# Kernel tuning notes

Hardware: AMD Instinct MI355X
Metric: run time of the kernel (lower is better)

The kernel has to match this reference:

```python
import jax, jax.numpy as jnp
import numpy as np

N_EMBD = 1024
N_HEAD = 16
R = 16
SCALING = 1.0 / 16.0  # loralib default lora_alpha=1, scaling = alpha/r


def lora_linear(x, W, b, A, B):
    # loralib: y = x @ W.T + b + (x @ A.T) @ B.T * scaling
    return x @ W.T + b + (x @ A.T) @ B.T * SCALING


def setup_inputs() -> dict:
    key = jax.random.key(0)
    ks = jax.random.split(key, 16)
    B, T, S, C = 8, 1024, 256, N_EMBD
    std = 0.02
    return {
        "x": jax.random.normal(ks[0], (B, T, C), jnp.float32),
        "feature": jax.random.normal(ks[1], (B, S, C), jnp.float32),
        # c_attn (q projection)
        "Wq": jax.random.normal(ks[2], (C, C), jnp.float32) * std,
        "bq": jnp.zeros((C,), jnp.float32),
        "Aq": jax.random.normal(ks[3], (R, C), jnp.float32) * std,
        "Bq": jnp.zeros((C, R), jnp.float32),
        # feature_attn (kv projection)
        "Wf": jax.random.normal(ks[4], (2 * C, C), jnp.float32) * std,
        "bf": jnp.zeros((2 * C,), jnp.float32),
        "Af": jax.random.normal(ks[5], (R, C), jnp.float32) * std,
        "Bf": jnp.zeros((2 * C, R), jnp.float32),
        # c_proj
        "Wp": jax.random.normal(ks[6], (C, C), jnp.float32) * std,
        "bp": jnp.zeros((C,), jnp.float32),
        "Ap": jax.random.normal(ks[7], (R, C), jnp.float32) * std,
        "Bp": jnp.zeros((C, R), jnp.float32),
    }


def reference(x, feature, Wq, bq, Aq, Bq, Wf, bf, Af, Bf, Wp, bp, Ap, Bp):
    Bsz, T, C = x.shape
    S = feature.shape[1]
    H = N_HEAD
    D = C // H

    q = lora_linear(x, Wq, bq, Aq, Bq).reshape(Bsz, T, H, D).transpose(0, 2, 1, 3)
    kv = lora_linear(feature, Wf, bf, Af, Bf)
    k, v = kv[..., :C], kv[..., C:]
    k = k.reshape(Bsz, S, H, D).transpose(0, 2, 1, 3)
    v = v.reshape(Bsz, S, H, D).transpose(0, 2, 1, 3)

    att = jnp.einsum("bhtd,bhsd->bhts", q, k) * (1.0 / np.sqrt(D))
    mask = jnp.tril(jnp.ones((T, S), bool))  # bias[:, :, :T, :S]
    att = jnp.where(mask, att, -jnp.inf)
    att = jax.nn.softmax(att, axis=-1)

    y = jnp.einsum("bhts,bhsd->bhtd", att, v)
    y = y.transpose(0, 2, 1, 3).reshape(Bsz, T, C)
    return lora_linear(y, Wp, bp, Ap, Bp)
```

## Files before the change

kernel.cpp:

```cpp
#include <hip/hip_runtime.h>
#include <hip/hip_bf16.h>
#include <stdint.h>
#include <stddef.h>

typedef __hip_bfloat16 bf16;
typedef __attribute__((ext_vector_type(8))) short short8;
typedef __attribute__((ext_vector_type(4))) float floatx4;

__device__ __forceinline__ void async_load16(const bf16* g, bf16* l) {
#if defined(__has_builtin) && __has_builtin(__builtin_amdgcn_global_load_lds)
  __builtin_amdgcn_global_load_lds((__attribute__((address_space(1))) void*)g,
                                   (__attribute__((address_space(3))) void*)l,
                                   16, 0, 0);
#else
  *(short8*)l = *(const short8*)g;
#endif
}

__device__ __forceinline__ int wave_detect_f32(const unsigned short* __restrict__ xr) {
  const int lane = threadIdx.x & 63;
  const unsigned short u = xr[lane];
  const int e = (u >> 7) & 0xFF;
  const unsigned long long m = __ballot(e >= 0x93);
  return (__popcll(m) > 5) ? 1 : 0;
}

__device__ __forceinline__ float ldf(const void* p, int i, int flg) {
  return flg ? ((const float*)p)[i] : __bfloat162float(((const bf16*)p)[i]);
}

struct PrepArgs {
  const void *x, *ft, *bq, *bf, *bp;
  const void *Wq, *Aq, *Bq, *Wf, *Af, *Bf, *Wp, *Ap, *Bp;
  bf16 *cx, *cft, *cbq, *cbf, *cbp, *weffq, *wefff, *weffp;
};

__device__ __forceinline__ void canon4(const void* src, bf16* dst, int i4, int flg) {
  if (flg) {
    const float4 v = ((const float4*)src)[i4];
    dst[i4 * 4 + 0] = __float2bfloat16(v.x);
    dst[i4 * 4 + 1] = __float2bfloat16(v.y);
    dst[i4 * 4 + 2] = __float2bfloat16(v.z);
    dst[i4 * 4 + 3] = __float2bfloat16(v.w);
  } else {
    ((uint2*)dst)[i4] = ((const uint2*)src)[i4];
  }
}

__device__ __forceinline__ void weff1(const void* W, const void* Bm, const void* Am,
                                      bf16* dst, int idx, int flg) {
  const int n = idx >> 10, k = idx & 1023;
  float acc = 0.f;
#pragma unroll
  for (int r = 0; r < 16; ++r)
    acc += ldf(Bm, n * 16 + r, flg) * ldf(Am, r * 1024 + k, flg);
  dst[idx] = __float2bfloat16(ldf(W, idx, flg) + 0.0625f * acc);
}

__global__ __launch_bounds__(256) void prep_kernel(PrepArgs a) {
  const int flg = wave_detect_f32((const unsigned short*)a.x);
  const int bid = blockIdx.x, tid = threadIdx.x;
  if (bid < 8192) {
    canon4(a.x, a.cx, bid * 256 + tid, flg);
  } else if (bid < 10240) {
    canon4(a.ft, a.cft, (bid - 8192) * 256 + tid, flg);
  } else if (bid < 10241) {
    canon4(a.bq, a.cbq, tid, flg);
  } else if (bid < 10243) {
    canon4(a.bf, a.cbf, (bid - 10241) * 256 + tid, flg);
  } else if (bid < 10244) {
    canon4(a.bp, a.cbp, tid, flg);
  } else if (bid < 14340) {
    weff1(a.Wq, a.Bq, a.Aq, a.weffq, (bid - 10244) * 256 + tid, flg);
  } else if (bid < 22532) {
    weff1(a.Wf, a.Bf, a.Af, a.wefff, (bid - 14340) * 256 + tid, flg);
  } else {
    weff1(a.Wp, a.Bp, a.Ap, a.weffp, (bid - 22532) * 256 + tid, flg);
  }
}

__global__ __launch_bounds__(256) void gemm_qkv(
    const bf16* __restrict__ cx, const bf16* __restrict__ cft,
    const bf16* __restrict__ weffq, const bf16* __restrict__ wefff,
    const bf16* __restrict__ cbq, const bf16* __restrict__ cbf,
    bf16* __restrict__ qws, bf16* __restrict__ kws, bf16* __restrict__ vtws) {
  __shared__ __align__(16) bf16 sA[128 * 32];
  __shared__ __align__(16) bf16 sB[128 * 32];
  const int bid = blockIdx.x, tid = threadIdx.x;
  const int K = 1024;
  int mode, bm, bn;
  const bf16 *A, *Bt, *bias;
  if (bid < 512) {
    mode = 0; A = cx; Bt = weffq; bias = cbq;
    bm = (((bid & 7) << 3) | ((bid >> 3) & 7)) * 128;
    bn = (bid >> 6) * 128;
  } else {
    const int b2 = bid - 512;
    mode = 1; A = cft; Bt = wefff; bias = cbf;
    bm = (((b2 & 7) << 1) | ((b2 >> 3) & 1)) * 128;
    bn = (b2 >> 4) * 128;
  }
  const int srow = tid >> 2;
  const int scol = ((tid & 3) ^ (srow & 3)) << 3;
  const bf16* ga0 = A + (size_t)(bm + srow) * K + scol;
  const bf16* ga1 = ga0 + (size_t)64 * K;
  const bf16* gb0 = Bt + (size_t)(bn + srow) * K + scol;
  const bf16* gb1 = gb0 + (size_t)64 * K;
  bf16* lA0 = sA + tid * 8;
  bf16* lA1 = sA + 2048 + tid * 8;
  bf16* lB0 = sB + tid * 8;
  bf16* lB1 = sB + 2048 + tid * 8;
  const int wave = tid >> 6, lane = tid & 63;
  const int wm = (wave >> 1) << 6, wn = (wave & 1) << 6;
  const int lrow = lane & 15, quad = lane >> 4;
  const int swz = ((quad ^ (lrow & 3)) << 3);

  const floatx4 zero4 = {0.f, 0.f, 0.f, 0.f};
  floatx4 acc[4][4];
#pragma unroll
  for (int i = 0; i < 4; ++i)
#pragma unroll
    for (int j = 0; j < 4; ++j) acc[i][j] = zero4;

  for (int k0 = 0; k0 < K; k0 += 32) {
    async_load16(ga0, lA0);
    async_load16(ga1, lA1);
    async_load16(gb0, lB0);
    async_load16(gb1, lB1);
    ga0 += 32; ga1 += 32; gb0 += 32; gb1 += 32;
    __syncthreads();
    short8 af[4], bfr[4];
#pragma unroll
    for (int i = 0; i < 4; ++i) {
      af[i]  = *(const short8*)(sA + (wm + i * 16 + lrow) * 32 + swz);
      bfr[i] = *(const short8*)(sB + (wn + i * 16 + lrow) * 32 + swz);
    }
#pragma unroll
    for (int i = 0; i < 4; ++i)
#pragma unroll
      for (int j = 0; j < 4; ++j)
        acc[i][j] = __builtin_amdgcn_mfma_f32_16x16x32_bf16(af[i], bfr[j], acc[i][j], 0, 0, 0);
    __syncthreads();
  }

#pragma unroll
  for (int i = 0; i < 4; ++i) {
    const int mbase = bm + wm + i * 16 + quad * 4;
#pragma unroll
    for (int j = 0; j < 4; ++j) {
      const int n = bn + wn + j * 16 + lrow;
      const float bv = __bfloat162float(bias[n]);
#pragma unroll
      for (int r = 0; r < 4; ++r) {
        const int m = mbase + r;
        const bf16 hval = __float2bfloat16(acc[i][j][r] + bv);
        if (mode == 0) {
          const int b = m >> 10, t = m & 1023, hh = n >> 6, d = n & 63;
          qws[(((size_t)(b * 16 + hh)) * 1024 + t) * 64 + d] = hval;
        } else {
          const int b = m >> 8, s = m & 255;
          if (n < 1024) {
            const int hh = n >> 6, d = n & 63;
            kws[(((size_t)(b * 16 + hh)) * 256 + s) * 64 + d] = hval;
          } else {
            const int nn = n - 1024, hh = nn >> 6, d = nn & 63;
            vtws[(((size_t)(b * 16 + hh)) * 64 + d) * 256 + s] = hval;
          }
        }
      }
    }
  }
}

__global__ __launch_bounds__(256) void gemm_out(
    const bf16* __restrict__ A, const bf16* __restrict__ Bt,
    const bf16* __restrict__ bias, void* __restrict__ out0,
    const unsigned short* __restrict__ xraw) {
  __shared__ __align__(16) bf16 sA[128 * 32];
  __shared__ __align__(16) bf16 sB[128 * 32];
  const int bid = blockIdx.x, tid = threadIdx.x;
  const int K = 1024, N = 1024;
  const int bm = (((bid & 7) << 3) | ((bid >> 3) & 7)) * 128;
  const int bn = (bid >> 6) * 128;
  const int srow = tid >> 2;
  const int scol = ((tid & 3) ^ (srow & 3)) << 3;
  const bf16* ga0 = A + (size_t)(bm + srow) * K + scol;
  const bf16* ga1 = ga0 + (size_t)64 * K;
  const bf16* gb0 = Bt + (size_t)(bn + srow) * K + scol;
  const bf16* gb1 = gb0 + (size_t)64 * K;
  bf16* lA0 = sA + tid * 8;
  bf16* lA1 = sA + 2048 + tid * 8;
  bf16* lB0 = sB + tid * 8;
  bf16* lB1 = sB + 2048 + tid * 8;
  const int wave = tid >> 6, lane = tid & 63;
  const int wm = (wave >> 1) << 6, wn = (wave & 1) << 6;
  const int lrow = lane & 15, quad = lane >> 4;
  const int swz = ((quad ^ (lrow & 3)) << 3);

  const floatx4 zero4 = {0.f, 0.f, 0.f, 0.f};
  floatx4 acc[4][4];
#pragma unroll
  for (int i = 0; i < 4; ++i)
#pragma unroll
    for (int j = 0; j < 4; ++j) acc[i][j] = zero4;

  for (int k0 = 0; k0 < K; k0 += 32) {
    async_load16(ga0, lA0);
    async_load16(ga1, lA1);
    async_load16(gb0, lB0);
    async_load16(gb1, lB1);
    ga0 += 32; ga1 += 32; gb0 += 32; gb1 += 32;
    __syncthreads();
    short8 af[4], bfr[4];
#pragma unroll
    for (int i = 0; i < 4; ++i) {
      af[i]  = *(const short8*)(sA + (wm + i * 16 + lrow) * 32 + swz);
      bfr[i] = *(const short8*)(sB + (wn + i * 16 + lrow) * 32 + swz);
    }
#pragma unroll
    for (int i = 0; i < 4; ++i)
#pragma unroll
      for (int j = 0; j < 4; ++j)
        acc[i][j] = __builtin_amdgcn_mfma_f32_16x16x32_bf16(af[i], bfr[j], acc[i][j], 0, 0, 0);
    __syncthreads();
  }

  const int flg = wave_detect_f32(xraw);
#pragma unroll
  for (int i = 0; i < 4; ++i) {
    const int mbase = bm + wm + i * 16 + quad * 4;
#pragma unroll
    for (int j = 0; j < 4; ++j) {
      const int n = bn + wn + j * 16 + lrow;
      const float bv = __bfloat162float(bias[n]);
#pragma unroll
      for (int r = 0; r < 4; ++r) {
        const int m = mbase + r;
        const float fval = acc[i][j][r] + bv;
        const size_t idx = (size_t)m * N + n;
        if (flg) ((float*)out0)[idx] = fval;
        else     ((bf16*)out0)[idx] = __float2bfloat16(fval);
      }
    }
  }
}

#define SKP 72
#define SVP 264
__global__ __launch_bounds__(512, 2) void attn_kernel(
    const bf16* __restrict__ qws, const bf16* __restrict__ kws,
    const bf16* __restrict__ vtws, bf16* __restrict__ yws) {
  const int b = blockIdx.z, h = blockIdx.y, qc = blockIdx.x;
  const int bh = b * 16 + h;
  __shared__ __align__(16) bf16 sK[256 * SKP];
  __shared__ __align__(16) bf16 sVt[64 * SVP];
  __shared__ __align__(16) bf16 sP[8][16 * SVP];
  const int tid = threadIdx.x, wave = tid >> 6, lane = tid & 63;
  const int lrow = lane & 15, quad = lane >> 4;
  const bf16* kg = kws + (size_t)bh * (256 * 64);
  const bf16* vg = vtws + (size_t)bh * (64 * 256);
#pragma unroll
  for (int i = 0; i < 4; ++i) {
    const int idx = i * 512 + tid;
    const int kr = idx >> 3, kc = (idx & 7) * 8;
    *(short8*)(sK + kr * SKP + kc) = *(const short8*)(kg + kr * 64 + kc);
    const int vr = idx >> 5, vc = (idx & 31) * 8;
    *(short8*)(sVt + vr * SVP + vc) = *(const short8*)(vg + vr * 256 + vc);
  }
  __syncthreads();
  bf16* sPw = sP[wave];
  const floatx4 zero4 = {0.f, 0.f, 0.f, 0.f};
  const float kscale = 0.18033688011112042f;

  for (int st = 0; st < 4; ++st) {
    const int t0 = qc * 512 + wave * 64 + st * 16;
    const bf16* qrow = qws + ((size_t)bh * 1024 + t0 + lrow) * 64;
    const short8 aq0 = *(const short8*)(qrow + quad * 8);
    const short8 aq1 = *(const short8*)(qrow + 32 + quad * 8);
    floatx4 sc[16];
#pragma unroll
    for (int nt = 0; nt < 16; ++nt) {
      floatx4 c = zero4;
      c = __builtin_amdgcn_mfma_f32_16x16x32_bf16(
          aq0, *(const short8*)(sK + (nt * 16 + lrow) * SKP + quad * 8), c, 0, 0, 0);
      c = __builtin_amdgcn_mfma_f32_16x16x32_bf16(
          aq1, *(const short8*)(sK + (nt * 16 + lrow) * SKP + 32 + quad * 8), c, 0, 0, 0);
      sc[nt] = c;
    }
    float sum[4] = {0.f, 0.f, 0.f, 0.f};
#pragma unroll
    for (int nt = 0; nt < 16; ++nt) {
      const int s = nt * 16 + lrow;
#pragma unroll
      for (int r = 0; r < 4; ++r) {
        const int t = t0 + quad * 4 + r;
        const float p = (s <= t) ? exp2f(sc[nt][r] * kscale) : 0.f;
        sum[r] += p;
        sPw[(quad * 4 + r) * SVP + nt * 16 + lrow] = __float2bfloat16(p);
      }
    }
#pragma unroll
    for (int r = 0; r < 4; ++r) {
      sum[r] += __shfl_xor(sum[r], 1, 16);
      sum[r] += __shfl_xor(sum[r], 2, 16);
      sum[r] += __shfl_xor(sum[r], 4, 16);
      sum[r] += __shfl_xor(sum[r], 8, 16);
    }
    asm volatile("s_waitcnt lgkmcnt(0)" ::: "memory");
    floatx4 ya[4];
#pragma unroll
    for (int nt = 0; nt < 4; ++nt) ya[nt] = zero4;
#pragma unroll
    for (int ks = 0; ks < 8; ++ks) {
      const short8 ap = *(const short8*)(sPw + lrow * SVP + ks * 32 + quad * 8);
#pragma unroll
      for (int nt = 0; nt < 4; ++nt)
        ya[nt] = __builtin_amdgcn_mfma_f32_16x16x32_bf16(
            ap, *(const short8*)(sVt + (nt * 16 + lrow) * SVP + ks * 32 + quad * 8),
            ya[nt], 0, 0, 0);
    }
#pragma unroll
    for (int r = 0; r < 4; ++r) {
      const float rl = 1.f / sum[r];
      const int t = t0 + quad * 4 + r;
#pragma unroll
      for (int nt = 0; nt < 4; ++nt)
        yws[((size_t)b * 1024 + t) * 1024 + h * 64 + nt * 16 + lrow] =
            __float2bfloat16(ya[nt][r] * rl);
    }
  }
}

extern "C" void kernel_launch(void* const* d_in, const int* in_sizes, int n_in,
                              void* d_out, int out_size, void* d_ws, size_t ws_size,
                              hipStream_t stream) {
  char* p = (char*)d_ws;
  bf16* cbq   = (bf16*)p;     p += 4096;
  bf16* cbf   = (bf16*)p;     p += 8192;
  bf16* cbp   = (bf16*)p;     p += 4096;
  bf16* weffq = (bf16*)p;     p += (size_t)1024 * 1024 * 2;
  bf16* wefff = (bf16*)p;     p += (size_t)2048 * 1024 * 2;
  bf16* weffp = (bf16*)p;     p += (size_t)1024 * 1024 * 2;
  bf16* qws   = (bf16*)p;     p += (size_t)8 * 16 * 1024 * 64 * 2;
  bf16* kws   = (bf16*)p;     p += (size_t)8 * 16 * 256 * 64 * 2;
  bf16* vtws  = (bf16*)p;     p += (size_t)8 * 16 * 64 * 256 * 2;
  bf16* cft   = (bf16*)p;     p += (size_t)8 * 256 * 1024 * 2;
  bf16* cx    = (bf16*)p;     p += (size_t)8 * 1024 * 1024 * 2;
  bf16* yws   = cx;
  const size_t required = (size_t)(p - (char*)d_ws);
  if (ws_size < required) return;

  PrepArgs pa;
  pa.x = d_in[0]; pa.ft = d_in[1];
  pa.bq = d_in[3]; pa.bf = d_in[7]; pa.bp = d_in[11];
  pa.Wq = d_in[2];  pa.Aq = d_in[4];  pa.Bq = d_in[5];
  pa.Wf = d_in[6];  pa.Af = d_in[8];  pa.Bf = d_in[9];
  pa.Wp = d_in[10]; pa.Ap = d_in[12]; pa.Bp = d_in[13];
  pa.cx = cx; pa.cft = cft; pa.cbq = cbq; pa.cbf = cbf; pa.cbp = cbp;
  pa.weffq = weffq; pa.wefff = wefff; pa.weffp = weffp;
  prep_kernel<<<26628, 256, 0, stream>>>(pa);

  gemm_qkv<<<768, 256, 0, stream>>>(cx, cft, weffq, wefff, cbq, cbf, qws, kws, vtws);
  attn_kernel<<<dim3(2, 16, 8), 512, 0, stream>>>(qws, kws, vtws, yws);
  gemm_out<<<512, 256, 0, stream>>>(yws, weffp, cbp, d_out, (const unsigned short*)d_in[0]);
}
```

Measured before the change: 229.0 us.

## Rewrite GEMMs with 256x128 tiles, triple-buffered async LDS pipeline, 512 threads

Both projection GEMMs now share a core that uses 512-thread blocks computing 256x128 output tiles with a K-step of 64. Global-to-LDS async loads are triple-buffered, prefetching two stages ahead with explicit vmcnt waits and raw barriers, and MFMA issue is raised with setprio. The aim is to hide global load latency behind MFMA work and to get more reuse per LDS tile than the earlier single-buffered 128x128, K=32 loop. In exchange it uses far more LDS (about 144 KB per block), which limits occupancy, and it relies on hand-tuned waitcnt counts that must match the load counts exactly.

```diff
diff --git a/kernel.cpp b/kernel.cpp
--- a/kernel.cpp
+++ b/kernel.cpp
@@ -79,41 +79,103 @@
   }
 }
 
-__global__ __launch_bounds__(256) void gemm_qkv(
+#define GSLOT ((256 + 128) * 64)
+
+__device__ __forceinline__ void stage_slot(const bf16* __restrict__ gA,
+                                           const bf16* __restrict__ gB,
+                                           bf16* slot, int tid) {
+#pragma unroll
+  for (int l = 0; l < 4; ++l) {
+    const int D = l * 512 + tid;
+    const int r = D >> 3;
+    const int c = (D & 7) ^ (r & 7);
+    async_load16(gA + (size_t)r * 1024 + c * 8, slot + D * 8);
+  }
+#pragma unroll
+  for (int l = 0; l < 2; ++l) {
+    const int D = l * 512 + tid;
+    const int r = D >> 3;
+    const int c = (D & 7) ^ (r & 7);
+    async_load16(gB + (size_t)r * 1024 + c * 8, slot + 256 * 64 + D * 8);
+  }
+}
+
+__device__ __forceinline__ void gemm_core(const bf16* __restrict__ A,
+                                          const bf16* __restrict__ Bt,
+                                          int bm, int bn, bf16* sT,
+                                          floatx4 (&acc)[4][4]) {
+  const int tid = threadIdx.x;
+  const int wave = tid >> 6, lane = tid & 63;
+  const int lrow = lane & 15, quad = lane >> 4;
+  const int wm64 = (wave >> 1) << 6;
+  const int wn64 = (wave & 1) << 6;
+  const int pc0 = (quad ^ (lrow & 7)) << 3;
+
+  const bf16* gA = A + (size_t)bm * 1024;
+  const bf16* gB = Bt + (size_t)bn * 1024;
+
+  stage_slot(gA, gB, sT, tid);
+  stage_slot(gA + 64, gB + 64, sT + GSLOT, tid);
+
+#pragma unroll
+  for (int t = 0; t < 16; ++t) {
+    asm volatile("s_waitcnt lgkmcnt(0)" ::: "memory");
+    __builtin_amdgcn_s_barrier();
+    __builtin_amdgcn_sched_barrier(0);
+    if (t < 14) {
+      stage_slot(gA + (t + 2) * 64, gB + (t + 2) * 64,
+                 sT + ((t + 2) % 3) * GSLOT, tid);
+      asm volatile("s_waitcnt vmcnt(12)" ::: "memory");
+    } else if (t == 14) {
+      asm volatile("s_waitcnt vmcnt(6)" ::: "memory");
+    } else {
+      asm volatile("s_waitcnt vmcnt(0)" ::: "memory");
+    }
+    __builtin_amdgcn_s_barrier();
+    __builtin_amdgcn_sched_barrier(0);
+
+    const bf16* slotA = sT + (t % 3) * GSLOT;
+    const bf16* slotB = slotA + 256 * 64;
+    short8 a_[4][2], b_[4][2];
+#pragma unroll
+    for (int i = 0; i < 4; ++i) {
+      const bf16* ra = slotA + (wm64 + i * 16 + lrow) * 64;
+      a_[i][0] = *(const short8*)(ra + pc0);
+      a_[i][1] = *(const short8*)(ra + (pc0 ^ 32));
+      const bf16* rb = slotB + (wn64 + i * 16 + lrow) * 64;
+      b_[i][0] = *(const short8*)(rb + pc0);
+      b_[i][1] = *(const short8*)(rb + (pc0 ^ 32));
+    }
+    __builtin_amdgcn_s_setprio(1);
+#pragma unroll
+    for (int kh = 0; kh < 2; ++kh)
+#pragma unroll
+      for (int i = 0; i < 4; ++i)
+#pragma unroll
+        for (int j = 0; j < 4; ++j)
+          acc[i][j] = __builtin_amdgcn_mfma_f32_16x16x32_bf16(
+              a_[i][kh], b_[j][kh], acc[i][j], 0, 0, 0);
+    __builtin_amdgcn_s_setprio(0);
+  }
+}
+
+__global__ __launch_bounds__(512, 2) void gemm_qkv(
     const bf16* __restrict__ cx, const bf16* __restrict__ cft,
     const bf16* __restrict__ weffq, const bf16* __restrict__ wefff,
     const bf16* __restrict__ cbq, const bf16* __restrict__ cbf,
     bf16* __restrict__ qws, bf16* __restrict__ kws, bf16* __restrict__ vtws) {
-  __shared__ __align__(16) bf16 sA[128 * 32];
-  __shared__ __align__(16) bf16 sB[128 * 32];
-  const int bid = blockIdx.x, tid = threadIdx.x;
-  const int K = 1024;
+  __shared__ __align__(16) bf16 sT[3 * GSLOT];
+  const int bid = blockIdx.x;
   int mode, bm, bn;
   const bf16 *A, *Bt, *bias;
-  if (bid < 512) {
+  if (bid < 256) {
     mode = 0; A = cx; Bt = weffq; bias = cbq;
-    bm = (((bid & 7) << 3) | ((bid >> 3) & 7)) * 128;
-    bn = (bid >> 6) * 128;
+    bm = (bid >> 3) * 256; bn = (bid & 7) * 128;
   } else {
-    const int b2 = bid - 512;
+    const int b2 = bid - 256;
     mode = 1; A = cft; Bt = wefff; bias = cbf;
-    bm = (((b2 & 7) << 1) | ((b2 >> 3) & 1)) * 128;
-    bn = (b2 >> 4) * 128;
-  }
-  const int srow = tid >> 2;
-  const int scol = ((tid & 3) ^ (srow & 3)) << 3;
-  const bf16* ga0 = A + (size_t)(bm + srow) * K + scol;
-  const bf16* ga1 = ga0 + (size_t)64 * K;
-  const bf16* gb0 = Bt + (size_t)(bn + srow) * K + scol;
-  const bf16* gb1 = gb0 + (size_t)64 * K;
-  bf16* lA0 = sA + tid * 8;
-  bf16* lA1 = sA + 2048 + tid * 8;
-  bf16* lB0 = sB + tid * 8;
-  bf16* lB1 = sB + 2048 + tid * 8;
-  const int wave = tid >> 6, lane = tid & 63;
-  const int wm = (wave >> 1) << 6, wn = (wave & 1) << 6;
-  const int lrow = lane & 15, quad = lane >> 4;
-  const int swz = ((quad ^ (lrow & 3)) << 3);
+    bm = (b2 >> 4) * 256; bn = (b2 & 15) * 128;
+  }
 
   const floatx4 zero4 = {0.f, 0.f, 0.f, 0.f};
   floatx4 acc[4][4];
@@ -122,33 +184,17 @@
 #pragma unroll
     for (int j = 0; j < 4; ++j) acc[i][j] = zero4;
 
-  for (int k0 = 0; k0 < K; k0 += 32) {
-    async_load16(ga0, lA0);
-    async_load16(ga1, lA1);
-    async_load16(gb0, lB0);
-    async_load16(gb1, lB1);
-    ga0 += 32; ga1 += 32; gb0 += 32; gb1 += 32;
-    __syncthreads();
-    short8 af[4], bfr[4];
-#pragma unroll
-    for (int i = 0; i < 4; ++i) {
-      af[i]  = *(const short8*)(sA + (wm + i * 16 + lrow) * 32 + swz);
-      bfr[i] = *(const short8*)(sB + (wn + i * 16 + lrow) * 32 + swz);
-    }
-#pragma unroll
-    for (int i = 0; i < 4; ++i)
-#pragma unroll
-      for (int j = 0; j < 4; ++j)
-        acc[i][j] = __builtin_amdgcn_mfma_f32_16x16x32_bf16(af[i], bfr[j], acc[i][j], 0, 0, 0);
-    __syncthreads();
-  }
-
+  gemm_core(A, Bt, bm, bn, sT, acc);
+
+  const int tid = threadIdx.x, wave = tid >> 6, lane = tid & 63;
+  const int lrow = lane & 15, quad = lane >> 4;
+  const int wm64 = (wave >> 1) << 6, wn64 = (wave & 1) << 6;
 #pragma unroll
   for (int i = 0; i < 4; ++i) {
-    const int mbase = bm + wm + i * 16 + quad * 4;
+    const int mbase = bm + wm64 + i * 16 + quad * 4;
 #pragma unroll
     for (int j = 0; j < 4; ++j) {
-      const int n = bn + wn + j * 16 + lrow;
+      const int n = bn + wn64 + j * 16 + lrow;
       const float bv = __bfloat162float(bias[n]);
 #pragma unroll
       for (int r = 0; r < 4; ++r) {
@@ -172,30 +218,14 @@
   }
 }
 
-__global__ __launch_bounds__(256) void gemm_out(
+__global__ __launch_bounds__(512, 2) void gemm_out(
     const bf16* __restrict__ A, const bf16* __restrict__ Bt,
     const bf16* __restrict__ bias, void* __restrict__ out0,
     const unsigned short* __restrict__ xraw) {
-  __shared__ __align__(16) bf16 sA[128 * 32];
-  __shared__ __align__(16) bf16 sB[128 * 32];
-  const int bid = blockIdx.x, tid = threadIdx.x;
-  const int K = 1024, N = 1024;
-  const int bm = (((bid & 7) << 3) | ((bid >> 3) & 7)) * 128;
-  const int bn = (bid >> 6) * 128;
-  const int srow = tid >> 2;
-  const int scol = ((tid & 3) ^ (srow & 3)) << 3;
-  const bf16* ga0 = A + (size_t)(bm + srow) * K + scol;
-  const bf16* ga1 = ga0 + (size_t)64 * K;
-  const bf16* gb0 = Bt + (size_t)(bn + srow) * K + scol;
-  const bf16* gb1 = gb0 + (size_t)64 * K;
-  bf16* lA0 = sA + tid * 8;
-  bf16* lA1 = sA + 2048 + tid * 8;
-  bf16* lB0 = sB + tid * 8;
-  bf16* lB1 = sB + 2048 + tid * 8;
-  const int wave = tid >> 6, lane = tid & 63;
-  const int wm = (wave >> 1) << 6, wn = (wave & 1) << 6;
-  const int lrow = lane & 15, quad = lane >> 4;
-  const int swz = ((quad ^ (lrow & 3)) << 3);
+  __shared__ __align__(16) bf16 sT[3 * GSLOT];
+  const int bid = blockIdx.x;
+  const int bm = (bid >> 3) * 256, bn = (bid & 7) * 128;
+  const int N = 1024;
 
   const floatx4 zero4 = {0.f, 0.f, 0.f, 0.f};
   floatx4 acc[4][4];
@@ -204,34 +234,18 @@
 #pragma unroll
     for (int j = 0; j < 4; ++j) acc[i][j] = zero4;
 
-  for (int k0 = 0; k0 < K; k0 += 32) {
-    async_load16(ga0, lA0);
-    async_load16(ga1, lA1);
-    async_load16(gb0, lB0);
-    async_load16(gb1, lB1);
-    ga0 += 32; ga1 += 32; gb0 += 32; gb1 += 32;
-    __syncthreads();
-    short8 af[4], bfr[4];
-#pragma unroll
-    for (int i = 0; i < 4; ++i) {
-      af[i]  = *(const short8*)(sA + (wm + i * 16 + lrow) * 32 + swz);
-      bfr[i] = *(const short8*)(sB + (wn + i * 16 + lrow) * 32 + swz);
-    }
-#pragma unroll
-    for (int i = 0; i < 4; ++i)
-#pragma unroll
-      for (int j = 0; j < 4; ++j)
-        acc[i][j] = __builtin_amdgcn_mfma_f32_16x16x32_bf16(af[i], bfr[j], acc[i][j], 0, 0, 0);
-    __syncthreads();
-  }
-
+  gemm_core(A, Bt, bm, bn, sT, acc);
+
+  const int tid = threadIdx.x, wave = tid >> 6, lane = tid & 63;
+  const int lrow = lane & 15, quad = lane >> 4;
+  const int wm64 = (wave >> 1) << 6, wn64 = (wave & 1) << 6;
   const int flg = wave_detect_f32(xraw);
 #pragma unroll
   for (int i = 0; i < 4; ++i) {
-    const int mbase = bm + wm + i * 16 + quad * 4;
+    const int mbase = bm + wm64 + i * 16 + quad * 4;
 #pragma unroll
     for (int j = 0; j < 4; ++j) {
-      const int n = bn + wn + j * 16 + lrow;
+      const int n = bn + wn64 + j * 16 + lrow;
       const float bv = __bfloat162float(bias[n]);
 #pragma unroll
       for (int r = 0; r < 4; ++r) {
@@ -360,7 +374,7 @@
   pa.weffq = weffq; pa.wefff = wefff; pa.weffp = weffp;
   prep_kernel<<<26628, 256, 0, stream>>>(pa);
 
-  gemm_qkv<<<768, 256, 0, stream>>>(cx, cft, weffq, wefff, cbq, cbf, qws, kws, vtws);
+  gemm_qkv<<<384, 512, 0, stream>>>(cx, cft, weffq, wefff, cbq, cbf, qws, kws, vtws);
   attn_kernel<<<dim3(2, 16, 8), 512, 0, stream>>>(qws, kws, vtws, yws);
-  gemm_out<<<512, 256, 0, stream>>>(yws, weffp, cbp, d_out, (const unsigned short*)d_in[0]);
-}
+  gemm_out<<<256, 512, 0, stream>>>(yws, weffp, cbp, d_out, (const unsigned short*)d_in[0]);
+}
```

Result: slower. 241.1 us (+5.3%).
